# Kernel optimization log

Hardware: AMD Instinct MI355X
Metric: run time of the kernel (lower is better)

## Reference

```python
import jax, jax.numpy as jnp
import numpy as np
import math

B, S, D, H, L = 256, 256, 256, 4, 2
DH = D // H
NITEMS = 50000
EPS = 1e-5


def setup_inputs() -> dict:
    key = jax.random.key(0)
    ks = jax.random.split(key, 16)
    w = lambda k, shape, scale: (jax.random.normal(k, shape, jnp.float32) * scale)
    return {
        "input_ids": jax.random.randint(ks[0], (B, S), 0, NITEMS),
        "item_emb": w(ks[1], (NITEMS, D), 0.02),
        "pos_emb": w(ks[2], (S, D), 0.02),
        "Wq": w(ks[3], (L, D, D), 0.05),
        "bq": jnp.zeros((L, D), jnp.float32),
        "Wk": w(ks[4], (L, D, D), 0.05),
        "bk": jnp.zeros((L, D), jnp.float32),
        "Wv": w(ks[5], (L, D, D), 0.05),
        "bv": jnp.zeros((L, D), jnp.float32),
        "Wo": w(ks[6], (L, D, D), 0.05),
        "bo": jnp.zeros((L, D), jnp.float32),
        "W1": w(ks[7], (L, D, 4 * D), 0.05),
        "b1": jnp.zeros((L, 4 * D), jnp.float32),
        "W2": w(ks[8], (L, 4 * D, D), 0.05),
        "b2": jnp.zeros((L, D), jnp.float32),
    }


def _layer_norm(x):
    mu = jnp.mean(x, axis=-1, keepdims=True)
    var = jnp.mean(jnp.square(x - mu), axis=-1, keepdims=True)
    return (x - mu) * jax.lax.rsqrt(var + EPS)


def reference(input_ids, item_emb, pos_emb, Wq, bq, Wk, bk, Wv, bv,
              Wo, bo, W1, b1, W2, b2):
    Bn, Sn = input_ids.shape
    dtype = item_emb.dtype
    # attention bias: padding (id>0) AND causal; (1-mask)*-10000
    pad = (input_ids > 0).astype(dtype)                       # [B,S]
    causal = jnp.tril(jnp.ones((Sn, Sn), dtype))              # [S,S]
    mask = pad[:, None, None, :] * causal[None, None]         # [B,1,S,S]
    attn_bias = (1.0 - mask) * -10000.0

    # input embedding (dropout is identity in eval)
    x = _layer_norm(item_emb[input_ids] + pos_emb[None])      # [B,S,D]
    total = x
    scale = 1.0 / math.sqrt(DH)

    for l in range(L):
        # --- self-attention ---
        def heads(z):  # [B,S,D] -> [B,H,S,DH]
            return z.reshape(Bn, Sn, H, DH).transpose(0, 2, 1, 3)
        q = heads(x @ Wq[l] + bq[l])
        k = heads(x @ Wk[l] + bk[l])
        v = heads(x @ Wv[l] + bv[l])
        scores = jnp.einsum('bhqd,bhkd->bhqk', q, k) * scale + attn_bias
        probs = jax.nn.softmax(scores, axis=-1)
        ctx = jnp.einsum('bhqk,bhkd->bhqd', probs, v)
        ctx = ctx.transpose(0, 2, 1, 3).reshape(Bn, Sn, D)
        h = _layer_norm(ctx @ Wo[l] + bo[l] + x)
        # --- FFN (no residual in IntermediateLayer) ---
        ffn = jax.nn.gelu(h @ W1[l] + b1[l], approximate=False) @ W2[l] + b2[l]
        x = _layer_norm(ffn)
        total = total + x

    return total
```

## Files before the change

### kernel.cpp

```cpp
#include <hip/hip_runtime.h>
#include <math.h>

typedef __attribute__((ext_vector_type(8))) short short8;
typedef __attribute__((ext_vector_type(4))) short shortx4;
typedef __attribute__((ext_vector_type(4))) float floatx4;

#define BQ 256
#define SQ 256
#define DQ 256
#define HQ 4

__device__ __forceinline__ short f2bf(float f) {
  union { float f; unsigned u; } c; c.f = f;
  unsigned r = c.u + 0x7fffu + ((c.u >> 16) & 1u);
  return (short)(r >> 16);
}
__device__ __forceinline__ float bf2f(short s) {
  union { unsigned u; float f; } c; c.u = ((unsigned)(unsigned short)s) << 16;
  return c.f;
}
__device__ __forceinline__ float gelu_fast(float x) {
  float t = x * (0.7978845608f + 0.0356774081f * x * x);
  return x / (1.0f + __expf(-2.0f * t));
}
__device__ __forceinline__ void async16(const void* g, void* l) {
  __builtin_amdgcn_global_load_lds(
      (const __attribute__((address_space(1))) void*)g,
      (__attribute__((address_space(3))) void*)l, 16, 0, 0);
}

__global__ __launch_bounds__(256) void wtrans_kernel(
    const float* __restrict__ Wq, const float* __restrict__ Wk, const float* __restrict__ Wv,
    const float* __restrict__ Wo, const float* __restrict__ W1, const float* __restrict__ W2,
    const float* __restrict__ bq, const float* __restrict__ bk, const float* __restrict__ bv,
    short* __restrict__ WqkvT, short* __restrict__ WoT, short* __restrict__ W1T,
    short* __restrict__ W2T, float* __restrict__ bqkv) {
  const int bid = blockIdx.x, tid = threadIdx.x;
  if (bid >= 384) {
    int i = bid - 384;
    int l = i / 3, which = i - l * 3;
    const float* src = (which == 0) ? bq : ((which == 1) ? bk : bv);
    bqkv[l * 768 + which * 256 + tid] = src[l * 256 + tid];
    return;
  }
  __shared__ float t[64][65];
  const float* src; short* dst; int K, N, tile;
  if (bid < 96)       { int l = bid / 48, r = bid % 48, which = r / 16; tile = r % 16;
    src = ((which == 0) ? Wq : (which == 1) ? Wk : Wv) + l * 65536;
    dst = WqkvT + (l * 3 + which) * 65536; K = 256; N = 256; }
  else if (bid < 128) { int i = bid - 96, l = i / 16; tile = i % 16;
    src = Wo + l * 65536; dst = WoT + l * 65536; K = 256; N = 256; }
  else if (bid < 256) { int i = bid - 128, l = i / 64; tile = i % 64;
    src = W1 + l * 262144; dst = W1T + l * 262144; K = 256; N = 1024; }
  else                { int i = bid - 256, l = i / 64; tile = i % 64;
    src = W2 + l * 262144; dst = W2T + l * 262144; K = 1024; N = 256; }
  const int ntj = N >> 6;
  const int ti = tile / ntj, tj = tile - ti * ntj;
  {
    int r = tid >> 2, c0 = (tid & 3) * 16;
    const float* sp = src + (size_t)(ti * 64 + r) * N + tj * 64 + c0;
#pragma unroll
    for (int j = 0; j < 4; ++j) {
      floatx4 v = *(const floatx4*)(sp + j * 4);
      t[r][c0 + j * 4 + 0] = v[0]; t[r][c0 + j * 4 + 1] = v[1];
      t[r][c0 + j * 4 + 2] = v[2]; t[r][c0 + j * 4 + 3] = v[3];
    }
  }
  __syncthreads();
  {
    int d = tid & 63, ch = tid >> 6;
    short8 o[2];
#pragma unroll
    for (int j = 0; j < 16; ++j) o[j >> 3][j & 7] = f2bf(t[ch * 16 + j][d]);
    short* dp = dst + (size_t)(tj * 64 + d) * K + ti * 64 + ch * 16;
    *(short8*)dp = o[0];
    *(short8*)(dp + 8) = o[1];
  }
}

__global__ __launch_bounds__(256) void embed_kernel(const int* __restrict__ ids,
    const float* __restrict__ item, const float* __restrict__ pos,
    short* __restrict__ xb, float* __restrict__ tot) {
  const int tid = threadIdx.x, lane = tid & 63, w = tid >> 6;
  const int row = blockIdx.x * 4 + w;
  const int s = row & (SQ - 1);
  const int id = ids[row];
  floatx4 a = *(const floatx4*)(item + (size_t)id * DQ + lane * 4);
  floatx4 p = *(const floatx4*)(pos + (size_t)s * DQ + lane * 4);
  float v[4];
#pragma unroll
  for (int i = 0; i < 4; ++i) v[i] = a[i] + p[i];
  float sm = v[0] + v[1] + v[2] + v[3];
  float ss = v[0]*v[0] + v[1]*v[1] + v[2]*v[2] + v[3]*v[3];
#pragma unroll
  for (int off = 32; off; off >>= 1) { sm += __shfl_xor(sm, off); ss += __shfl_xor(ss, off); }
  float mu = sm * (1.0f / DQ);
  float var = ss * (1.0f / DQ) - mu * mu;
  float rs = rsqrtf(var + 1e-5f);
  shortx4 o; floatx4 y;
#pragma unroll
  for (int i = 0; i < 4; ++i) { y[i] = (v[i] - mu) * rs; o[i] = f2bf(y[i]); }
  *(shortx4*)(xb + (size_t)row * DQ + lane * 4) = o;
  *(floatx4*)(tot + (size_t)row * DQ + lane * 4) = y;
}

template <int ACT, int LN, int RES, int TOT, int SMODE>
__global__ __launch_bounds__(512, 4) void gemm_kernel(
    const short* __restrict__ A, const short* __restrict__ Bt,
    const float* __restrict__ bias, const short* __restrict__ res,
    short* __restrict__ out, float* __restrict__ tot, short* __restrict__ vt,
    int M, int N, int K) {
  __shared__ short smem[26624];
  float* redS  = (float*)(smem + 24576);
  float* redS2 = redS + 512;
  const int tid = threadIdx.x, lane = tid & 63, w = tid >> 6;
  const int lane15 = lane & 15, quad = lane >> 4;
  const int wm = w & 1, wn = w >> 1;
  const int bm = blockIdx.y, bn = blockIdx.x;

  const int rA = lane >> 2;
  const int swzA = (rA & 3) ^ ((rA >> 2) & 3);
  const int gA = ((lane & 3) ^ swzA) * 8;
  const short* Ag  = A  + (size_t)(bm * 128 + w * 16 + rA) * K + gA;
  const short* Bg0 = Bt + (size_t)(bn * 256 + w * 32 + rA) * K + gA;
  const short* Bg1 = Bg0 + (size_t)16 * K;
  const int qs = ((quad ^ ((lane15 & 3) ^ ((lane15 >> 2) & 3))) * 8);

  floatx4 acc[4][4] = {};
  const int nk = K >> 5;
#define GSTG(kb_)                                                        \
  do {                                                                   \
    short* As_ = smem + (((kb_) & 1) * 12288);                           \
    async16(Ag  + (kb_) * 32, &As_[w * 512]);                            \
    async16(Bg0 + (kb_) * 32, &As_[4096 + w * 1024]);                    \
    async16(Bg1 + (kb_) * 32, &As_[4096 + w * 1024 + 512]);              \
  } while (0)

  GSTG(0);
  for (int kb = 0; kb < nk; ++kb) {
    __syncthreads();
    if (kb + 1 < nk) GSTG(kb + 1);
    const short* Asb = smem + ((kb & 1) * 12288);
    const short* Bsb = Asb + 4096;
    short8 af[4], bfr[4];
#pragma unroll
    for (int i = 0; i < 4; ++i) {
      af[i]  = *(const short8*)&Asb[(wm * 64 + i * 16 + lane15) * 32 + qs];
      bfr[i] = *(const short8*)&Bsb[(wn * 64 + i * 16 + lane15) * 32 + qs];
    }
#pragma unroll
    for (int i = 0; i < 4; ++i)
#pragma unroll
      for (int j = 0; j < 4; ++j)
        acc[i][j] = __builtin_amdgcn_mfma_f32_16x16x32_bf16(bfr[j], af[i], acc[i][j], 0, 0, 0);
  }
#undef GSTG

  float sum_[4], sq_[4];
#pragma unroll
  for (int i = 0; i < 4; ++i) { sum_[i] = 0.0f; sq_[i] = 0.0f; }
#pragma unroll
  for (int i = 0; i < 4; ++i) {
    size_t rowg = (size_t)bm * 128 + wm * 64 + i * 16 + lane15;
#pragma unroll
    for (int j = 0; j < 4; ++j) {
      int nloc = wn * 64 + j * 16 + quad * 4;
      floatx4 b4 = *(const floatx4*)(bias + bn * 256 + nloc);
      shortx4 r4;
      if (RES) r4 = *(const shortx4*)(res + rowg * 256 + nloc);
#pragma unroll
      for (int r = 0; r < 4; ++r) {
        float z = acc[i][j][r] + b4[r];
        if (RES) z += bf2f(r4[r]);
        if (ACT) z = gelu_fast(z);
        acc[i][j][r] = z;
        if (LN) { sum_[i] += z; sq_[i] += z * z; }
      }
    }
  }

  if (LN) {
#pragma unroll
    for (int i = 0; i < 4; ++i) {
      sum_[i] += __shfl_xor(sum_[i], 16); sum_[i] += __shfl_xor(sum_[i], 32);
      sq_[i]  += __shfl_xor(sq_[i], 16);  sq_[i]  += __shfl_xor(sq_[i], 32);
    }
    if (quad == 0) {
#pragma unroll
      for (int i = 0; i < 4; ++i) {
        int lr = wm * 64 + i * 16 + lane15;
        redS[lr * 4 + wn] = sum_[i];
        redS2[lr * 4 + wn] = sq_[i];
      }
    }
    __syncthreads();
#pragma unroll
    for (int i = 0; i < 4; ++i) {
      int lr = wm * 64 + i * 16 + lane15;
      float s = redS[lr * 4] + redS[lr * 4 + 1] + redS[lr * 4 + 2] + redS[lr * 4 + 3];
      float q = redS2[lr * 4] + redS2[lr * 4 + 1] + redS2[lr * 4 + 2] + redS2[lr * 4 + 3];
      float mu = s * (1.0f / 256.0f);
      float var = q * (1.0f / 256.0f) - mu * mu;
      float rs = rsqrtf(var + 1e-5f);
      size_t rowg = (size_t)bm * 128 + wm * 64 + i * 16 + lane15;
#pragma unroll
      for (int j = 0; j < 4; ++j) {
        int nloc = wn * 64 + j * 16 + quad * 4;
        floatx4 y;
#pragma unroll
        for (int r = 0; r < 4; ++r) y[r] = (acc[i][j][r] - mu) * rs;
        acc[i][j] = y;
        if (TOT) {
          floatx4* tp = (floatx4*)(tot + rowg * 256 + nloc);
          floatx4 t = *tp;
#pragma unroll
          for (int r = 0; r < 4; ++r) t[r] += y[r];
          *tp = t;
        }
      }
    }
  }

#pragma unroll
  for (int i = 0; i < 4; ++i) {
    __syncthreads();
    int lr = wm * 16 + lane15;
#pragma unroll
    for (int j = 0; j < 4; ++j) {
      shortx4 o;
#pragma unroll
      for (int r = 0; r < 4; ++r) o[r] = f2bf(acc[i][j][r]);
      *(shortx4*)&smem[lr * 264 + wn * 64 + j * 16 + quad * 4] = o;
    }
    __syncthreads();
    if (SMODE == 1 && bn == 2) {
      int d = tid & 255;
      int grp = tid >> 8;
      short vv[16];
#pragma unroll
      for (int rr = 0; rr < 16; ++rr) vv[rr] = smem[(grp * 16 + rr) * 264 + d];
      size_t row = ((size_t)((bm >> 1) * 256 + d)) * 256 + (bm & 1) * 128 + grp * 64 + i * 16;
      *(short8*)(vt + row) = *(short8*)&vv[0];
      *(short8*)(vt + row + 8) = *(short8*)&vv[8];
    } else {
#pragma unroll
      for (int it = 0; it < 2; ++it) {
        int t2 = tid + it * 512;
        int lr2 = t2 >> 5, c = (t2 & 31) * 8;
        short8 v = *(const short8*)&smem[lr2 * 264 + c];
        size_t rowg = (size_t)bm * 128 + (lr2 >> 4) * 64 + i * 16 + (lr2 & 15);
        short* dst = (SMODE == 1) ? out + (size_t)bn * M * 256 + rowg * 256 + c
                                  : out + rowg * (size_t)N + bn * 256 + c;
        *(short8*)dst = v;
      }
    }
  }
}

__global__ __launch_bounds__(512, 4) void attn_kernel(
    const short* __restrict__ qg, const short* __restrict__ kg,
    const short* __restrict__ vtg, const int* __restrict__ ids,
    short* __restrict__ ctxg) {
  __shared__ short lds[25088];
  float* padS = (float*)&lds[24576];
  const int tid = threadIdx.x, lane = tid & 63, w = tid >> 6;
  const int lane15 = lane & 15, quad = lane >> 4, l7 = lane15 & 7;
  const int h = blockIdx.x & 3, b = blockIdx.x >> 2;

  if (tid < 256) padS[tid] = (ids[b * 256 + tid] > 0) ? 0.0f : -10000.0f;

  const int stA[2] = {w, 15 - w};
  short8 qf[2][2];
#pragma unroll
  for (int tt = 0; tt < 2; ++tt) {
    int q0 = stA[tt] * 16;
#pragma unroll
    for (int ks = 0; ks < 2; ++ks)
      qf[tt][ks] = *(const short8*)(qg + (size_t)(b * 256 + q0 + lane15) * 256 +
                                    h * 64 + ks * 32 + quad * 8);
  }

  float m_[2][4], l_[2][4];
  floatx4 o[2][4];
#pragma unroll
  for (int tt = 0; tt < 2; ++tt)
#pragma unroll
    for (int r = 0; r < 4; ++r) {
      m_[tt][r] = -1e30f; l_[tt][r] = 0.0f;
#pragma unroll
      for (int dt = 0; dt < 4; ++dt) o[tt][dt][r] = 0.0f;
    }

  const int srow = tid >> 3;
  const int g8 = ((tid & 7) ^ (srow & 7)) * 8;
  const short* kgp = kg + (size_t)(b * 256 + srow) * 256 + h * 64 + g8;
  const short* vgp = vtg + (size_t)(b * 256 + h * 64 + srow) * 256 + g8;
  short* pbuf = &lds[16384 + w * 1024];

#define STG(kb_, ib_)                                                     \
  do {                                                                    \
    async16(kgp + (size_t)(kb_) * 64 * 256, &lds[(ib_) * 4096 + w * 512]);\
    async16(vgp + (kb_) * 64, &lds[8192 + (ib_) * 4096 + w * 512]);       \
  } while (0)

  STG(0, 0);

  for (int kb = 0; kb < 4; ++kb) {
    __syncthreads();
    if (kb < 3) STG(kb + 1, (kb + 1) & 1);
    const short* kbuf = &lds[(kb & 1) * 4096];
    const short* vbuf = &lds[8192 + (kb & 1) * 4096];

#pragma unroll
    for (int tt = 0; tt < 2; ++tt) {
      const int st = stA[tt];
      if (st < 4 * kb) continue;
      const int q0 = st * 16;
      const int diag = (st >> 2) == kb;
      const int stlo = st & 3;
      floatx4 e[4];
#pragma unroll
      for (int t16 = 0; t16 < 4; ++t16) {
        if (diag && t16 > stlo) {
          e[t16] = (floatx4){-1e30f, -1e30f, -1e30f, -1e30f};
          continue;
        }
        floatx4 a = {0.f, 0.f, 0.f, 0.f};
#pragma unroll
        for (int ks = 0; ks < 2; ++ks) {
          short8 kf = *(const short8*)&kbuf[(t16 * 16 + lane15) * 64 +
                                            (((ks * 4 + quad) ^ l7) * 8)];
          a = __builtin_amdgcn_mfma_f32_16x16x32_bf16(qf[tt][ks], kf, a, 0, 0, 0);
        }
        float pb = padS[kb * 64 + t16 * 16 + lane15];
        if (diag && t16 == stlo) {
          int kk = kb * 64 + t16 * 16 + lane15;
#pragma unroll
          for (int r = 0; r < 4; ++r)
            e[t16][r] = a[r] * 0.125f + ((kk <= q0 + quad * 4 + r) ? pb : -10000.0f);
        } else {
#pragma unroll
          for (int r = 0; r < 4; ++r) e[t16][r] = a[r] * 0.125f + pb;
        }
      }
#pragma unroll
      for (int r = 0; r < 4; ++r) {
        float mx = fmaxf(fmaxf(e[0][r], e[1][r]), fmaxf(e[2][r], e[3][r]));
        mx = fmaxf(mx, __shfl_xor(mx, 1)); mx = fmaxf(mx, __shfl_xor(mx, 2));
        mx = fmaxf(mx, __shfl_xor(mx, 4)); mx = fmaxf(mx, __shfl_xor(mx, 8));
        float mn = fmaxf(m_[tt][r], mx);
        float alpha = __expf(m_[tt][r] - mn);
        m_[tt][r] = mn;
        float s = 0.0f;
#pragma unroll
        for (int t16 = 0; t16 < 4; ++t16) {
          float ev = __expf(e[t16][r] - mn);
          e[t16][r] = ev; s += ev;
        }
        s += __shfl_xor(s, 1); s += __shfl_xor(s, 2);
        s += __shfl_xor(s, 4); s += __shfl_xor(s, 8);
        l_[tt][r] = l_[tt][r] * alpha + s;
#pragma unroll
        for (int dt = 0; dt < 4; ++dt) o[tt][dt][r] *= alpha;
        int qloc = quad * 4 + r;
        int swq = (qloc & 7) ^ (qloc >> 2);
#pragma unroll
        for (int t16 = 0; t16 < 4; ++t16) {
          int slot = (t16 * 2 + (lane15 >> 3)) ^ swq;
          pbuf[qloc * 64 + slot * 8 + l7] = f2bf(e[t16][r]);
        }
      }
#pragma unroll
      for (int kb2 = 0; kb2 < 2; ++kb2) {
        short8 pf = *(const short8*)&pbuf[lane15 * 64 +
                      (((kb2 * 4 + quad) ^ l7 ^ (lane15 >> 2)) * 8)];
#pragma unroll
        for (int dt = 0; dt < 4; ++dt) {
          short8 vf = *(const short8*)&vbuf[(dt * 16 + lane15) * 64 +
                        (((kb2 * 4 + quad) ^ l7) * 8)];
          o[tt][dt] = __builtin_amdgcn_mfma_f32_16x16x32_bf16(pf, vf, o[tt][dt], 0, 0, 0);
        }
      }
    }
  }

#pragma unroll
  for (int tt = 0; tt < 2; ++tt) {
    const int q0 = stA[tt] * 16;
#pragma unroll
    for (int r = 0; r < 4; ++r) {
      int qloc = quad * 4 + r;
      float inv = 1.0f / l_[tt][r];
#pragma unroll
      for (int dt = 0; dt < 4; ++dt)
        pbuf[qloc * 64 + ((dt ^ quad) * 16) + lane15] = f2bf(o[tt][dt][r] * inv);
    }
#pragma unroll
    for (int it = 0; it < 2; ++it) {
      int idx = it * 64 + lane;
      int row = idx >> 3, u = idx & 7;
      int d0 = (((u >> 1) ^ (row >> 2)) << 4) + (u & 1) * 8;
      short8 v = *(const short8*)&pbuf[row * 64 + u * 8];
      *(short8*)(ctxg + (size_t)(b * 256 + q0 + row) * 256 + h * 64 + d0) = v;
    }
  }
}

extern "C" void kernel_launch(void* const* d_in, const int* in_sizes, int n_in,
                              void* d_out, int out_size, void* d_ws, size_t ws_size,
                              hipStream_t stream) {
  const int*   ids  = (const int*)d_in[0];
  const float* item = (const float*)d_in[1];
  const float* pos  = (const float*)d_in[2];
  const float* Wq = (const float*)d_in[3];  const float* bq = (const float*)d_in[4];
  const float* Wk = (const float*)d_in[5];  const float* bk = (const float*)d_in[6];
  const float* Wv = (const float*)d_in[7];  const float* bv = (const float*)d_in[8];
  const float* Wo = (const float*)d_in[9];  const float* bo = (const float*)d_in[10];
  const float* W1 = (const float*)d_in[11]; const float* b1 = (const float*)d_in[12];
  const float* W2 = (const float*)d_in[13]; const float* b2 = (const float*)d_in[14];
  float* out = (float*)d_out;

  const size_t EL = (size_t)BQ * SQ * DQ;
  short* qb    = (short*)d_ws;
  short* kb_   = qb + EL;
  short* vt    = kb_ + EL;
  short* ctxb  = vt + EL;
  short* gb    = qb;
  short* xb    = ctxb + EL;
  short* hb    = xb + EL;
  short* WqkvT = hb + EL;
  short* WoT   = WqkvT + 2 * 3 * 65536;
  short* W1T   = WoT + 2 * 65536;
  short* W2T   = W1T + 2 * 262144;
  float* bqkv  = (float*)(W2T + 2 * 262144);

  const int M = BQ * SQ;

  wtrans_kernel<<<390, 256, 0, stream>>>(Wq, Wk, Wv, Wo, W1, W2, bq, bk, bv,
                                         WqkvT, WoT, W1T, W2T, bqkv);
  embed_kernel<<<M / 4, 256, 0, stream>>>(ids, item, pos, xb, out);

  for (int l = 0; l < 2; ++l) {
    gemm_kernel<0, 0, 0, 0, 1><<<dim3(3, M / 128), 512, 0, stream>>>(
        xb, WqkvT + (size_t)l * 3 * 65536, bqkv + l * 768, nullptr, qb, nullptr, vt,
        M, 768, 256);
    attn_kernel<<<BQ * HQ, 512, 0, stream>>>(qb, kb_, vt, ids, ctxb);
    gemm_kernel<0, 1, 1, 0, 0><<<dim3(1, M / 128), 512, 0, stream>>>(
        ctxb, WoT + (size_t)l * 65536, bo + l * 256, xb, hb, nullptr, nullptr,
        M, 256, 256);
    gemm_kernel<1, 0, 0, 0, 0><<<dim3(4, M / 128), 512, 0, stream>>>(
        hb, W1T + (size_t)l * 262144, b1 + l * 1024, nullptr, gb, nullptr, nullptr,
        M, 1024, 256);
    gemm_kernel<0, 1, 0, 1, 0><<<dim3(1, M / 128), 512, 0, stream>>>(
        gb, W2T + (size_t)l * 262144, b2 + l * 256, nullptr, xb, out, nullptr,
        M, 256, 1024);
  }
}
```

Measured before the change: 802.7 us.

## Triple-buffer async global-to-LDS loads in GEMM and attention kernels

Moves the GEMM and attention kernels from double to triple buffering of async global-to-LDS loads. Plain __syncthreads are replaced with explicit vmcnt waits and a raw barrier, so up to two stages of loads stay in flight while MFMA work runs. The aim is to hide global memory latency better. The cost is more LDS per block, which could cut occupancy, and hand-tuned waitcnt values that must match the number of outstanding loads for results to stay correct.

```diff
diff --git a/kernel.cpp b/kernel.cpp
--- a/kernel.cpp
+++ b/kernel.cpp
@@ -28,6 +28,10 @@
       (const __attribute__((address_space(1))) void*)g,
       (__attribute__((address_space(3))) void*)l, 16, 0, 0);
 }
+
+#define VM_WAIT(n) asm volatile("s_waitcnt vmcnt(" #n ")" ::: "memory")
+#define LGKM_WAIT0() asm volatile("s_waitcnt lgkmcnt(0)" ::: "memory")
+#define RAW_BAR() do { __builtin_amdgcn_s_barrier(); __builtin_amdgcn_sched_barrier(0); } while (0)
 
 __global__ __launch_bounds__(256) void wtrans_kernel(
     const float* __restrict__ Wq, const float* __restrict__ Wk, const float* __restrict__ Wv,
@@ -110,7 +114,7 @@
     const float* __restrict__ bias, const short* __restrict__ res,
     short* __restrict__ out, float* __restrict__ tot, short* __restrict__ vt,
     int M, int N, int K) {
-  __shared__ short smem[26624];
+  __shared__ short smem[36864];
   float* redS  = (float*)(smem + 24576);
   float* redS2 = redS + 512;
   const int tid = threadIdx.x, lane = tid & 63, w = tid >> 6;
@@ -130,17 +134,19 @@
   const int nk = K >> 5;
 #define GSTG(kb_)                                                        \
   do {                                                                   \
-    short* As_ = smem + (((kb_) & 1) * 12288);                           \
+    short* As_ = smem + (((kb_) % 3) * 12288);                           \
     async16(Ag  + (kb_) * 32, &As_[w * 512]);                            \
     async16(Bg0 + (kb_) * 32, &As_[4096 + w * 1024]);                    \
     async16(Bg1 + (kb_) * 32, &As_[4096 + w * 1024 + 512]);              \
   } while (0)
 
-  GSTG(0);
+  GSTG(0); GSTG(1);
   for (int kb = 0; kb < nk; ++kb) {
-    __syncthreads();
-    if (kb + 1 < nk) GSTG(kb + 1);
-    const short* Asb = smem + ((kb & 1) * 12288);
+    if (kb < nk - 1) VM_WAIT(3);
+    else             VM_WAIT(0);
+    RAW_BAR();
+    if (kb + 2 < nk) GSTG(kb + 2);
+    const short* Asb = smem + ((kb % 3) * 12288);
     const short* Bsb = Asb + 4096;
     short8 af[4], bfr[4];
 #pragma unroll
@@ -261,8 +267,8 @@
     const short* __restrict__ qg, const short* __restrict__ kg,
     const short* __restrict__ vtg, const int* __restrict__ ids,
     short* __restrict__ ctxg) {
-  __shared__ short lds[25088];
-  float* padS = (float*)&lds[24576];
+  __shared__ short lds[33280];
+  float* padS = (float*)&lds[32768];
   const int tid = threadIdx.x, lane = tid & 63, w = tid >> 6;
   const int lane15 = lane & 15, quad = lane >> 4, l7 = lane15 & 7;
   const int h = blockIdx.x & 3, b = blockIdx.x >> 2;
@@ -295,21 +301,25 @@
   const int g8 = ((tid & 7) ^ (srow & 7)) * 8;
   const short* kgp = kg + (size_t)(b * 256 + srow) * 256 + h * 64 + g8;
   const short* vgp = vtg + (size_t)(b * 256 + h * 64 + srow) * 256 + g8;
-  short* pbuf = &lds[16384 + w * 1024];
-
-#define STG(kb_, ib_)                                                     \
-  do {                                                                    \
-    async16(kgp + (size_t)(kb_) * 64 * 256, &lds[(ib_) * 4096 + w * 512]);\
-    async16(vgp + (kb_) * 64, &lds[8192 + (ib_) * 4096 + w * 512]);       \
+  short* pbuf = &lds[24576 + w * 1024];
+
+#define STG(kb_)                                                               \
+  do {                                                                         \
+    async16(kgp + (size_t)(kb_) * 64 * 256, &lds[((kb_) % 3) * 4096 + w * 512]);\
+    async16(vgp + (kb_) * 64, &lds[12288 + ((kb_) % 3) * 4096 + w * 512]);     \
   } while (0)
 
-  STG(0, 0);
+  STG(0); STG(1); STG(2);
+  LGKM_WAIT0();
 
   for (int kb = 0; kb < 4; ++kb) {
-    __syncthreads();
-    if (kb < 3) STG(kb + 1, (kb + 1) & 1);
-    const short* kbuf = &lds[(kb & 1) * 4096];
-    const short* vbuf = &lds[8192 + (kb & 1) * 4096];
+    if (kb == 0)      VM_WAIT(4);
+    else if (kb == 3) VM_WAIT(0);
+    else              VM_WAIT(2);
+    RAW_BAR();
+    if (kb == 1) STG(3);
+    const short* kbuf = &lds[(kb % 3) * 4096];
+    const short* vbuf = &lds[12288 + (kb % 3) * 4096];
 
 #pragma unroll
     for (int tt = 0; tt < 2; ++tt) {
```

New measurement: 835.3 us. 1.04x slower.
